# Performance work log

Measured on AMD Instinct MI355X. Metric: run time of the kernel, lower is better.

## Reference

```python
import jax, jax.numpy as jnp
import numpy as np

H = 32  # hidden size (hardcoded in source module)

def setup_inputs() -> dict:
    key = jax.random.key(0)
    ks = jax.random.split(key, 7)
    s = 1.0 / np.sqrt(H)  # PyTorch LSTM/Linear init scale
    return {
        "x":    jax.random.normal(ks[0], (8192, 512, 1), dtype=jnp.float32),
        "W_ih": jax.random.uniform(ks[1], (4 * H, 1), minval=-s, maxval=s, dtype=jnp.float32),
        "W_hh": jax.random.uniform(ks[2], (4 * H, H), minval=-s, maxval=s, dtype=jnp.float32),
        "b_ih": jax.random.uniform(ks[3], (4 * H,), minval=-s, maxval=s, dtype=jnp.float32),
        "b_hh": jax.random.uniform(ks[4], (4 * H,), minval=-s, maxval=s, dtype=jnp.float32),
        "W_fc": jax.random.uniform(ks[5], (1, H), minval=-s, maxval=s, dtype=jnp.float32),
        "b_fc": jax.random.uniform(ks[6], (1,), minval=-s, maxval=s, dtype=jnp.float32),
    }

def reference(x, W_ih, W_hh, b_ih, b_hh, W_fc, b_fc):
    B = x.shape[0]
    # Precompute input projections for all timesteps: [B, T, 4H]
    xg = jnp.einsum('bti,gi->btg', x, W_ih) + (b_ih + b_hh)
    xg_t = jnp.swapaxes(xg, 0, 1)  # [T, B, 4H] for scan over time

    def step(carry, xgt):
        h, c = carry
        gates = xgt + h @ W_hh.T           # [B, 4H]
        i, f, g, o = jnp.split(gates, 4, axis=-1)  # PyTorch gate order i,f,g,o
        i = jax.nn.sigmoid(i)
        f = jax.nn.sigmoid(f)
        g = jnp.tanh(g)
        o = jax.nn.sigmoid(o)
        c = f * c + i * g
        h = o * jnp.tanh(c)
        return (h, c), None

    h0 = jnp.zeros((B, H), dtype=x.dtype)
    c0 = jnp.zeros((B, H), dtype=x.dtype)
    (h_last, _), _ = jax.lax.scan(step, (h0, c0), xg_t)
    # Final linear head on last timestep hidden state: [B, output_size]
    return h_last @ W_fc.T + b_fc
```

## Files before the change

kernel.cpp:

```cpp
#include <hip/hip_runtime.h>
#include <hip/hip_bf16.h>


#define TT 512
#define HH 32
#define L2E 1.44269504088896340736f

typedef short bf16x8 __attribute__((ext_vector_type(8)));
typedef float f32x4 __attribute__((ext_vector_type(4)));

__device__ __forceinline__ short f2bf(float f) {
    unsigned u = __float_as_uint(f);
    u = (u + 0x7FFFu + ((u >> 16) & 1u)) >> 16;
    return (short)u;
}
__device__ __forceinline__ float bf2f(short s) {
    return __uint_as_float(((unsigned)(unsigned short)s) << 16);
}
__device__ __forceinline__ float fastrcp(float x) { return __builtin_amdgcn_rcpf(x); }
__device__ __forceinline__ float exp2f_(float x) { return __builtin_amdgcn_exp2f(x); }

#define XROW 132

__launch_bounds__(256, 2)
__global__ void lstm_kernel(const float* __restrict__ x,
                            const float* __restrict__ W_ih,
                            const float* __restrict__ W_hh,
                            const float* __restrict__ b_ih,
                            const float* __restrict__ b_hh,
                            const float* __restrict__ W_fc,
                            const float* __restrict__ b_fc,
                            float* __restrict__ out) {
    __shared__ short hhp[2][512];
    __shared__ short hlp[2][512];
    __shared__ float xbuf[16 * XROW];

    const int tid  = threadIdx.x;
    const int lane = tid & 63;
    const int w    = tid >> 6;
    const int c    = lane & 15;
    const int q    = lane >> 4;
    const int base = blockIdx.x * 16;

    const int gate = c & 3;
    const float asc = (gate == 2) ? (2.0f * L2E) : (-L2E);
    const int wrow0 = gate * 32 + 8 * (c >> 2);
    bf16x8 wah[2], wal[2];
    #pragma unroll
    for (int tt = 0; tt < 2; ++tt) {
        const int t8 = 2 * w + tt;
        #pragma unroll
        for (int j = 0; j < 8; ++j) {
            const float wf = W_hh[(wrow0 + t8) * HH + 8 * q + j] * asc;
            const short hi = f2bf(wf);
            wah[tt][j] = hi;
            wal[tt][j] = f2bf(wf - bf2f(hi));
        }
    }

    float wihs[2][4];
    f32x4 bcs[2];
    #pragma unroll
    for (int tt = 0; tt < 2; ++tt) {
        const int u = 8 * q + 2 * w + tt;
        #pragma unroll
        for (int r = 0; r < 4; ++r) {
            const float sc = (r == 2) ? (2.0f * L2E) : (-L2E);
            wihs[tt][r] = W_ih[32 * r + u] * sc;
            bcs[tt][r]  = (b_ih[32 * r + u] + b_hh[32 * r + u]) * sc;
        }
    }

    #pragma unroll
    for (int i = tid; i < 512; i += 256) { hhp[0][i] = 0; hlp[0][i] = 0; }

    float cs[2] = {0.f, 0.f};

    const int xrow = tid >> 4;
    const int xj4  = (tid & 15) * 4;

    const int rdo = q * 128 + c * 8;
    const int wro = q * 128 + c * 8 + 2 * w;

    #define STEP(t, RP, WP)                                                   \
    {                                                                         \
        const bf16x8 bh = *(const bf16x8*)&hhp[RP][rdo];                      \
        const bf16x8 bl = *(const bf16x8*)&hlp[RP][rdo];                      \
        const float xc = xbuf[c * XROW + ((t) & 127)];                        \
        f32x4 acc[2];                                                         \
        _Pragma("unroll")                                                     \
        for (int tt = 0; tt < 2; ++tt) {                                      \
            f32x4 a = bcs[tt];                                                \
            a = __builtin_amdgcn_mfma_f32_16x16x32_bf16(wah[tt], bh, a, 0,0,0);\
            a = __builtin_amdgcn_mfma_f32_16x16x32_bf16(wah[tt], bl, a, 0,0,0);\
            a = __builtin_amdgcn_mfma_f32_16x16x32_bf16(wal[tt], bh, a, 0,0,0);\
            acc[tt] = a;                                                      \
        }                                                                     \
        float hv[2];                                                          \
        _Pragma("unroll")                                                     \
        for (int tt = 0; tt < 2; ++tt) {                                      \
            const float Ei = exp2f_(acc[tt][0] + wihs[tt][0] * xc);           \
            const float Ef = exp2f_(acc[tt][1] + wihs[tt][1] * xc);           \
            const float G  = exp2f_(acc[tt][2] + wihs[tt][2] * xc);           \
            const float Eo = exp2f_(acc[tt][3] + wihs[tt][3] * xc);           \
            const float aig = (1.f + Ei) * (G + 1.f);                         \
            const float af  = 1.f + Ef;                                       \
            const float num = cs[tt] * aig + (G - 1.f) * af;                  \
            const float cn  = num * fastrcp(af * aig);                        \
            cs[tt] = cn;                                                      \
            float yc = cn * (2.0f * L2E);                                     \
            yc = fminf(60.f, fmaxf(-60.f, yc));                               \
            const float C = exp2f_(yc);                                       \
            hv[tt] = (C - 1.f) * fastrcp((C + 1.f) * (1.f + Eo));             \
        }                                                                     \
        union { __hip_bfloat162 b; int i; } ph, pl;                           \
        ph.b = __float22bfloat162_rn(make_float2(hv[0], hv[1]));              \
        const float h0h = bf2f((short)(ph.i & 0xFFFF));                       \
        const float h1h = bf2f((short)((unsigned)ph.i >> 16));                \
        pl.b = __float22bfloat162_rn(make_float2(hv[0] - h0h, hv[1] - h1h));  \
        *(int*)&hhp[WP][wro] = ph.i;                                          \
        *(int*)&hlp[WP][wro] = pl.i;                                          \
        __syncthreads();                                                      \
    }

    for (int t = 0; t < TT; t += 2) {
        if ((t & 127) == 0) {
            #pragma unroll
            for (int s = 0; s < 2; ++s) {
                const float4 v = *(const float4*)&x[(base + xrow) * TT + t + xj4 + 64 * s];
                *(float4*)&xbuf[xrow * XROW + xj4 + 64 * s] = v;
            }
            __syncthreads();
        }
        STEP(t,     0, 1);
        STEP(t + 1, 1, 0);
    }

    if (tid < 16) {
        float s = b_fc[0];
        #pragma unroll
        for (int u = 0; u < 32; ++u) {
            const int off = (u >> 3) * 128 + tid * 8 + (u & 7);
            s += (bf2f(hhp[0][off]) + bf2f(hlp[0][off])) * W_fc[u];
        }
        out[base + tid] = s;
    }
}

extern "C" void kernel_launch(void* const* d_in, const int* in_sizes, int n_in,
                              void* d_out, int out_size, void* d_ws, size_t ws_size,
                              hipStream_t stream) {
    const float* x    = (const float*)d_in[0];
    const float* W_ih = (const float*)d_in[1];
    const float* W_hh = (const float*)d_in[2];
    const float* b_ih = (const float*)d_in[3];
    const float* b_hh = (const float*)d_in[4];
    const float* W_fc = (const float*)d_in[5];
    const float* b_fc = (const float*)d_in[6];
    float* out = (float*)d_out;

    const int B = 8192;
    lstm_kernel<<<B / 16, 256, 0, stream>>>(x, W_ih, W_hh, b_ih, b_hh,
                                            W_fc, b_fc, out);
}
```

Measured before the change: 282.9 us.

## Process two 16-row batch groups per block to interleave independent recurrences

Each block now handles 32 batch rows as two independent 16-row groups, issuing the MFMAs for both groups before the gate math. The aim is to give each wave two independent dependency chains per timestep, hiding MFMA and transcendental latency, while halving the number of __syncthreads per sequence row. Launch bounds drop to one block per CU-slot and the grid halves to 256 blocks, which lowers occupancy and may leave many CUs on a 256-CU part idle or underused.

```diff
diff --git a/kernel.cpp b/kernel.cpp
--- a/kernel.cpp
+++ b/kernel.cpp
@@ -21,8 +21,9 @@
 __device__ __forceinline__ float exp2f_(float x) { return __builtin_amdgcn_exp2f(x); }
 
 #define XROW 132
+#define XSZ  (16 * XROW)
 
-__launch_bounds__(256, 2)
+__launch_bounds__(256, 1)
 __global__ void lstm_kernel(const float* __restrict__ x,
                             const float* __restrict__ W_ih,
                             const float* __restrict__ W_hh,
@@ -31,16 +32,16 @@
                             const float* __restrict__ W_fc,
                             const float* __restrict__ b_fc,
                             float* __restrict__ out) {
-    __shared__ short hhp[2][512];
-    __shared__ short hlp[2][512];
-    __shared__ float xbuf[16 * XROW];
+    __shared__ short hhp[2][2][512];
+    __shared__ short hlp[2][2][512];
+    __shared__ float xbuf[2][XSZ];
 
     const int tid  = threadIdx.x;
     const int lane = tid & 63;
     const int w    = tid >> 6;
     const int c    = lane & 15;
     const int q    = lane >> 4;
-    const int base = blockIdx.x * 16;
+    const int base = blockIdx.x * 32;
 
     const int gate = c & 3;
     const float asc = (gate == 2) ? (2.0f * L2E) : (-L2E);
@@ -72,63 +73,79 @@
     }
 
     #pragma unroll
-    for (int i = tid; i < 512; i += 256) { hhp[0][i] = 0; hlp[0][i] = 0; }
+    for (int i = tid; i < 512; i += 256) {
+        hhp[0][0][i] = 0; hlp[0][0][i] = 0;
+        hhp[1][0][i] = 0; hlp[1][0][i] = 0;
+    }
 
-    float cs[2] = {0.f, 0.f};
-
-    const int xrow = tid >> 4;
-    const int xj4  = (tid & 15) * 4;
+    float cs[2][2] = {{0.f, 0.f}, {0.f, 0.f}};
 
     const int rdo = q * 128 + c * 8;
-    const int wro = q * 128 + c * 8 + 2 * w;
+    const int wro = rdo + 2 * w;
 
     #define STEP(t, RP, WP)                                                   \
     {                                                                         \
-        const bf16x8 bh = *(const bf16x8*)&hhp[RP][rdo];                      \
-        const bf16x8 bl = *(const bf16x8*)&hlp[RP][rdo];                      \
-        const float xc = xbuf[c * XROW + ((t) & 127)];                        \
-        f32x4 acc[2];                                                         \
+        bf16x8 bhv[2], blv[2];                                                \
+        float xc[2];                                                          \
         _Pragma("unroll")                                                     \
-        for (int tt = 0; tt < 2; ++tt) {                                      \
-            f32x4 a = bcs[tt];                                                \
-            a = __builtin_amdgcn_mfma_f32_16x16x32_bf16(wah[tt], bh, a, 0,0,0);\
-            a = __builtin_amdgcn_mfma_f32_16x16x32_bf16(wah[tt], bl, a, 0,0,0);\
-            a = __builtin_amdgcn_mfma_f32_16x16x32_bf16(wal[tt], bh, a, 0,0,0);\
-            acc[tt] = a;                                                      \
+        for (int g = 0; g < 2; ++g) {                                         \
+            bhv[g] = *(const bf16x8*)&hhp[g][RP][rdo];                        \
+            blv[g] = *(const bf16x8*)&hlp[g][RP][rdo];                        \
+            xc[g]  = xbuf[g][c * XROW + ((t) & 127)];                         \
         }                                                                     \
-        float hv[2];                                                          \
+        f32x4 acc[2][2];                                                      \
         _Pragma("unroll")                                                     \
-        for (int tt = 0; tt < 2; ++tt) {                                      \
-            const float Ei = exp2f_(acc[tt][0] + wihs[tt][0] * xc);           \
-            const float Ef = exp2f_(acc[tt][1] + wihs[tt][1] * xc);           \
-            const float G  = exp2f_(acc[tt][2] + wihs[tt][2] * xc);           \
-            const float Eo = exp2f_(acc[tt][3] + wihs[tt][3] * xc);           \
-            const float aig = (1.f + Ei) * (G + 1.f);                         \
-            const float af  = 1.f + Ef;                                       \
-            const float num = cs[tt] * aig + (G - 1.f) * af;                  \
-            const float cn  = num * fastrcp(af * aig);                        \
-            cs[tt] = cn;                                                      \
-            float yc = cn * (2.0f * L2E);                                     \
-            yc = fminf(60.f, fmaxf(-60.f, yc));                               \
-            const float C = exp2f_(yc);                                       \
-            hv[tt] = (C - 1.f) * fastrcp((C + 1.f) * (1.f + Eo));             \
+        for (int g = 0; g < 2; ++g) {                                         \
+            _Pragma("unroll")                                                 \
+            for (int tt = 0; tt < 2; ++tt) {                                  \
+                f32x4 a = bcs[tt];                                            \
+                a = __builtin_amdgcn_mfma_f32_16x16x32_bf16(wah[tt], bhv[g], a, 0,0,0); \
+                a = __builtin_amdgcn_mfma_f32_16x16x32_bf16(wah[tt], blv[g], a, 0,0,0); \
+                a = __builtin_amdgcn_mfma_f32_16x16x32_bf16(wal[tt], bhv[g], a, 0,0,0); \
+                acc[g][tt] = a;                                               \
+            }                                                                 \
         }                                                                     \
-        union { __hip_bfloat162 b; int i; } ph, pl;                           \
-        ph.b = __float22bfloat162_rn(make_float2(hv[0], hv[1]));              \
-        const float h0h = bf2f((short)(ph.i & 0xFFFF));                       \
-        const float h1h = bf2f((short)((unsigned)ph.i >> 16));                \
-        pl.b = __float22bfloat162_rn(make_float2(hv[0] - h0h, hv[1] - h1h));  \
-        *(int*)&hhp[WP][wro] = ph.i;                                          \
-        *(int*)&hlp[WP][wro] = pl.i;                                          \
+        _Pragma("unroll")                                                     \
+        for (int g = 0; g < 2; ++g) {                                         \
+            float hv[2];                                                      \
+            _Pragma("unroll")                                                 \
+            for (int tt = 0; tt < 2; ++tt) {                                  \
+                const float Ei = exp2f_(acc[g][tt][0] + wihs[tt][0] * xc[g]); \
+                const float Ef = exp2f_(acc[g][tt][1] + wihs[tt][1] * xc[g]); \
+                const float G  = exp2f_(acc[g][tt][2] + wihs[tt][2] * xc[g]); \
+                const float Eo = exp2f_(acc[g][tt][3] + wihs[tt][3] * xc[g]); \
+                const float aig = (1.f + Ei) * (G + 1.f);                     \
+                const float af  = 1.f + Ef;                                   \
+                const float num = cs[g][tt] * aig + (G - 1.f) * af;           \
+                const float cn  = num * fastrcp(af * aig);                    \
+                cs[g][tt] = cn;                                               \
+                float yc = cn * (2.0f * L2E);                                 \
+                yc = fminf(60.f, fmaxf(-60.f, yc));                           \
+                const float C = exp2f_(yc);                                   \
+                hv[tt] = (C - 1.f) * fastrcp((C + 1.f) * (1.f + Eo));         \
+            }                                                                 \
+            union { __hip_bfloat162 b; int i; } ph, pl;                       \
+            ph.b = __float22bfloat162_rn(make_float2(hv[0], hv[1]));          \
+            const float h0h = bf2f((short)(ph.i & 0xFFFF));                   \
+            const float h1h = bf2f((short)((unsigned)ph.i >> 16));            \
+            pl.b = __float22bfloat162_rn(make_float2(hv[0] - h0h, hv[1] - h1h)); \
+            *(int*)&hhp[g][WP][wro] = ph.i;                                   \
+            *(int*)&hlp[g][WP][wro] = pl.i;                                   \
+        }                                                                     \
         __syncthreads();                                                      \
     }
 
     for (int t = 0; t < TT; t += 2) {
         if ((t & 127) == 0) {
             #pragma unroll
-            for (int s = 0; s < 2; ++s) {
-                const float4 v = *(const float4*)&x[(base + xrow) * TT + t + xj4 + 64 * s];
-                *(float4*)&xbuf[xrow * XROW + xj4 + 64 * s] = v;
+            for (int s = 0; s < 4; ++s) {
+                const int lin = tid + 256 * s;
+                const int g   = lin >> 9;
+                const int row = (lin >> 5) & 15;
+                const int j4  = (lin & 31) * 4;
+                const float4 v =
+                    *(const float4*)&x[(base + g * 16 + row) * TT + t + j4];
+                *(float4*)&xbuf[g][row * XROW + j4] = v;
             }
             __syncthreads();
         }
@@ -136,14 +153,16 @@
         STEP(t + 1, 1, 0);
     }
 
-    if (tid < 16) {
+    if (tid < 32) {
+        const int g  = tid >> 4;
+        const int bb = tid & 15;
         float s = b_fc[0];
         #pragma unroll
         for (int u = 0; u < 32; ++u) {
-            const int off = (u >> 3) * 128 + tid * 8 + (u & 7);
-            s += (bf2f(hhp[0][off]) + bf2f(hlp[0][off])) * W_fc[u];
+            const int off = (u >> 3) * 128 + bb * 8 + (u & 7);
+            s += (bf2f(hhp[g][0][off]) + bf2f(hlp[g][0][off])) * W_fc[u];
         }
-        out[base + tid] = s;
+        out[base + g * 16 + bb] = s;
     }
 }
 
@@ -160,6 +179,6 @@
     float* out = (float*)d_out;
 
     const int B = 8192;
-    lstm_kernel<<<B / 16, 256, 0, stream>>>(x, W_ih, W_hh, b_ih, b_hh,
+    lstm_kernel<<<B / 32, 256, 0, stream>>>(x, W_ih, W_hh, b_ih, b_hh,
                                             W_fc, b_fc, out);
 }
```

Measured after the change: 322.8 us. +14.1%, slower.

## Split MFMA dependency chain and swizzle h write slots to avoid LDS bank conflicts

Applied to the files above, without the earlier changes.

The three chained MFMAs per gate tile become two independent chains: hi*hi from zero, and a second chain seeded with the input projection plus bias that adds the lo corrections. The two partial results are summed afterwards, which shortens the serial MFMA latency on the recurrent critical path and moves the x-projection FMA off the post-MFMA path. The hidden-state write offsets and the W_hh column order are XOR-swizzled by quad so the per-step 32-bit LDS writes spread across banks, and the final FC read uses the same permutation. The cost is extra vector adds and a slightly different floating-point summation order.

```diff
diff --git a/kernel.cpp b/kernel.cpp
--- a/kernel.cpp
+++ b/kernel.cpp
@@ -51,7 +51,8 @@
         const int t8 = 2 * w + tt;
         #pragma unroll
         for (int j = 0; j < 8; ++j) {
-            const float wf = W_hh[(wrow0 + t8) * HH + 8 * q + j] * asc;
+            const int u = 8 * q + (j ^ (2 * q));
+            const float wf = W_hh[(wrow0 + t8) * HH + u] * asc;
             const short hi = f2bf(wf);
             wah[tt][j] = hi;
             wal[tt][j] = f2bf(wf - bf2f(hi));
@@ -80,7 +81,7 @@
     const int xj4  = (tid & 15) * 4;
 
     const int rdo = q * 128 + c * 8;
-    const int wro = q * 128 + c * 8 + 2 * w;
+    const int wro = rdo + ((2 * w) ^ (2 * q));
 
     #define STEP(t, RP, WP)                                                   \
     {                                                                         \
@@ -90,19 +91,23 @@
         f32x4 acc[2];                                                         \
         _Pragma("unroll")                                                     \
         for (int tt = 0; tt < 2; ++tt) {                                      \
-            f32x4 a = bcs[tt];                                                \
-            a = __builtin_amdgcn_mfma_f32_16x16x32_bf16(wah[tt], bh, a, 0,0,0);\
-            a = __builtin_amdgcn_mfma_f32_16x16x32_bf16(wah[tt], bl, a, 0,0,0);\
-            a = __builtin_amdgcn_mfma_f32_16x16x32_bf16(wal[tt], bh, a, 0,0,0);\
-            acc[tt] = a;                                                      \
+            f32x4 ci;                                                         \
+            _Pragma("unroll")                                                 \
+            for (int r = 0; r < 4; ++r) ci[r] = wihs[tt][r] * xc + bcs[tt][r];\
+            f32x4 a1 = {0.f, 0.f, 0.f, 0.f};                                  \
+            a1 = __builtin_amdgcn_mfma_f32_16x16x32_bf16(wah[tt], bh, a1, 0,0,0);\
+            f32x4 a2 = __builtin_amdgcn_mfma_f32_16x16x32_bf16(wal[tt], bh, ci, 0,0,0);\
+            a2 = __builtin_amdgcn_mfma_f32_16x16x32_bf16(wah[tt], bl, a2, 0,0,0);\
+            _Pragma("unroll")                                                 \
+            for (int r = 0; r < 4; ++r) acc[tt][r] = a1[r] + a2[r];           \
         }                                                                     \
         float hv[2];                                                          \
         _Pragma("unroll")                                                     \
         for (int tt = 0; tt < 2; ++tt) {                                      \
-            const float Ei = exp2f_(acc[tt][0] + wihs[tt][0] * xc);           \
-            const float Ef = exp2f_(acc[tt][1] + wihs[tt][1] * xc);           \
-            const float G  = exp2f_(acc[tt][2] + wihs[tt][2] * xc);           \
-            const float Eo = exp2f_(acc[tt][3] + wihs[tt][3] * xc);           \
+            const float Ei = exp2f_(acc[tt][0]);                              \
+            const float Ef = exp2f_(acc[tt][1]);                              \
+            const float G  = exp2f_(acc[tt][2]);                              \
+            const float Eo = exp2f_(acc[tt][3]);                              \
             const float aig = (1.f + Ei) * (G + 1.f);                         \
             const float af  = 1.f + Ef;                                       \
             const float num = cs[tt] * aig + (G - 1.f) * af;                  \
@@ -140,7 +145,8 @@
         float s = b_fc[0];
         #pragma unroll
         for (int u = 0; u < 32; ++u) {
-            const int off = (u >> 3) * 128 + tid * 8 + (u & 7);
+            const int qb = u >> 3;
+            const int off = qb * 128 + tid * 8 + ((u & 7) ^ (2 * qb));
             s += (bf2f(hhp[0][off]) + bf2f(hlp[0][off])) * W_fc[u];
         }
         out[base + tid] = s;
```

Measured after the change: 290.4 us. 2.6% more time.

## Interleave two batch groups per block and use split fp16 MFMA recurrence

Applied to the files above, without the earlier changes.

Each block now handles 32 sequences as two 16-row groups whose time steps are staggered, so one group's gate nonlinearities overlap the other group's MFMA work. The recurrence switches from bf16 hi/lo with three MFMAs per tile to fp16 weights with a hi/lo split of h only, two MFMAs per tile. Each of 8 waves owns one tile instead of two. The x input is double-buffered across 128-step chunks, and an XOR swizzle is applied to the h writes to reduce LDS bank conflicts. The trade-off is lower weight precision (fp16 instead of bf16 hi+lo) and fewer, larger blocks.

```diff
diff --git a/kernel.cpp b/kernel.cpp
--- a/kernel.cpp
+++ b/kernel.cpp
@@ -1,28 +1,19 @@
 #include <hip/hip_runtime.h>
-#include <hip/hip_bf16.h>
 
 
 #define TT 512
 #define HH 32
 #define L2E 1.44269504088896340736f
 
-typedef short bf16x8 __attribute__((ext_vector_type(8)));
+typedef _Float16 f16x8 __attribute__((ext_vector_type(8)));
 typedef float f32x4 __attribute__((ext_vector_type(4)));
 
-__device__ __forceinline__ short f2bf(float f) {
-    unsigned u = __float_as_uint(f);
-    u = (u + 0x7FFFu + ((u >> 16) & 1u)) >> 16;
-    return (short)u;
-}
-__device__ __forceinline__ float bf2f(short s) {
-    return __uint_as_float(((unsigned)(unsigned short)s) << 16);
-}
 __device__ __forceinline__ float fastrcp(float x) { return __builtin_amdgcn_rcpf(x); }
 __device__ __forceinline__ float exp2f_(float x) { return __builtin_amdgcn_exp2f(x); }
 
 #define XROW 132
 
-__launch_bounds__(256, 2)
+__launch_bounds__(512)
 __global__ void lstm_kernel(const float* __restrict__ x,
                             const float* __restrict__ W_ih,
                             const float* __restrict__ W_hh,
@@ -31,119 +22,137 @@
                             const float* __restrict__ W_fc,
                             const float* __restrict__ b_fc,
                             float* __restrict__ out) {
-    __shared__ short hhp[2][512];
-    __shared__ short hlp[2][512];
-    __shared__ float xbuf[16 * XROW];
+    __shared__ _Float16 hh[2][512];
+    __shared__ _Float16 hl[2][512];
+    __shared__ float xbuf[2][2][16 * XROW];
 
     const int tid  = threadIdx.x;
     const int lane = tid & 63;
     const int w    = tid >> 6;
     const int c    = lane & 15;
     const int q    = lane >> 4;
-    const int base = blockIdx.x * 16;
+    const int base = blockIdx.x * 32;
 
     const int gate = c & 3;
     const float asc = (gate == 2) ? (2.0f * L2E) : (-L2E);
-    const int wrow0 = gate * 32 + 8 * (c >> 2);
-    bf16x8 wah[2], wal[2];
+    const int arow = gate * 32 + 8 * (c >> 2) + w;
+    f16x8 wah;
     #pragma unroll
-    for (int tt = 0; tt < 2; ++tt) {
-        const int t8 = 2 * w + tt;
-        #pragma unroll
-        for (int j = 0; j < 8; ++j) {
-            const float wf = W_hh[(wrow0 + t8) * HH + 8 * q + j] * asc;
-            const short hi = f2bf(wf);
-            wah[tt][j] = hi;
-            wal[tt][j] = f2bf(wf - bf2f(hi));
-        }
+    for (int j = 0; j < 8; ++j) {
+        const int u = 8 * q + (j ^ (2 * q));
+        wah[j] = (_Float16)(W_hh[arow * HH + u] * asc);
     }
 
-    float wihs[2][4];
-    f32x4 bcs[2];
+    const int uu = 8 * q + w;
+    f32x4 wihs, bcs;
     #pragma unroll
-    for (int tt = 0; tt < 2; ++tt) {
-        const int u = 8 * q + 2 * w + tt;
-        #pragma unroll
-        for (int r = 0; r < 4; ++r) {
-            const float sc = (r == 2) ? (2.0f * L2E) : (-L2E);
-            wihs[tt][r] = W_ih[32 * r + u] * sc;
-            bcs[tt][r]  = (b_ih[32 * r + u] + b_hh[32 * r + u]) * sc;
-        }
+    for (int r = 0; r < 4; ++r) {
+        const float sc = (r == 2) ? (2.0f * L2E) : (-L2E);
+        wihs[r] = W_ih[32 * r + uu] * sc;
+        bcs[r]  = (b_ih[32 * r + uu] + b_hh[32 * r + uu]) * sc;
     }
 
-    #pragma unroll
-    for (int i = tid; i < 512; i += 256) { hhp[0][i] = 0; hlp[0][i] = 0; }
+    hh[0][tid] = (_Float16)0.f; hl[0][tid] = (_Float16)0.f;
+    hh[1][tid] = (_Float16)0.f; hl[1][tid] = (_Float16)0.f;
 
-    float cs[2] = {0.f, 0.f};
+    float csA = 0.f, csB = 0.f;
 
-    const int xrow = tid >> 4;
-    const int xj4  = (tid & 15) * 4;
+    const float xB0 = x[(base + 16 + c) * TT + 0];
+    f32x4 accB = wihs * xB0 + bcs;
+    f32x4 accA;
 
     const int rdo = q * 128 + c * 8;
-    const int wro = q * 128 + c * 8 + 2 * w;
+    const int wro = rdo + (w ^ (2 * q));
 
-    #define STEP(t, RP, WP)                                                   \
-    {                                                                         \
-        const bf16x8 bh = *(const bf16x8*)&hhp[RP][rdo];                      \
-        const bf16x8 bl = *(const bf16x8*)&hlp[RP][rdo];                      \
-        const float xc = xbuf[c * XROW + ((t) & 127)];                        \
-        f32x4 acc[2];                                                         \
-        _Pragma("unroll")                                                     \
-        for (int tt = 0; tt < 2; ++tt) {                                      \
-            f32x4 a = bcs[tt];                                                \
-            a = __builtin_amdgcn_mfma_f32_16x16x32_bf16(wah[tt], bh, a, 0,0,0);\
-            a = __builtin_amdgcn_mfma_f32_16x16x32_bf16(wah[tt], bl, a, 0,0,0);\
-            a = __builtin_amdgcn_mfma_f32_16x16x32_bf16(wal[tt], bh, a, 0,0,0);\
-            acc[tt] = a;                                                      \
-        }                                                                     \
-        float hv[2];                                                          \
-        _Pragma("unroll")                                                     \
-        for (int tt = 0; tt < 2; ++tt) {                                      \
-            const float Ei = exp2f_(acc[tt][0] + wihs[tt][0] * xc);           \
-            const float Ef = exp2f_(acc[tt][1] + wihs[tt][1] * xc);           \
-            const float G  = exp2f_(acc[tt][2] + wihs[tt][2] * xc);           \
-            const float Eo = exp2f_(acc[tt][3] + wihs[tt][3] * xc);           \
+    const int xrow = tid >> 5;
+    const int xj4  = (tid & 31) * 4;
+
+    #define CELL(ACC, CS, H)                                                  \
+        {                                                                     \
+            const float Ei = exp2f_(ACC[0]);                                  \
+            const float Ef = exp2f_(ACC[1]);                                  \
+            const float G  = exp2f_(ACC[2]);                                  \
+            const float Eo = exp2f_(ACC[3]);                                  \
             const float aig = (1.f + Ei) * (G + 1.f);                         \
             const float af  = 1.f + Ef;                                       \
-            const float num = cs[tt] * aig + (G - 1.f) * af;                  \
-            const float cn  = num * fastrcp(af * aig);                        \
-            cs[tt] = cn;                                                      \
+            const float cn  = (CS * aig + (G - 1.f) * af) * fastrcp(af * aig);\
+            CS = cn;                                                          \
             float yc = cn * (2.0f * L2E);                                     \
             yc = fminf(60.f, fmaxf(-60.f, yc));                               \
             const float C = exp2f_(yc);                                       \
-            hv[tt] = (C - 1.f) * fastrcp((C + 1.f) * (1.f + Eo));             \
-        }                                                                     \
-        union { __hip_bfloat162 b; int i; } ph, pl;                           \
-        ph.b = __float22bfloat162_rn(make_float2(hv[0], hv[1]));              \
-        const float h0h = bf2f((short)(ph.i & 0xFFFF));                       \
-        const float h1h = bf2f((short)((unsigned)ph.i >> 16));                \
-        pl.b = __float22bfloat162_rn(make_float2(hv[0] - h0h, hv[1] - h1h));  \
-        *(int*)&hhp[WP][wro] = ph.i;                                          \
-        *(int*)&hlp[WP][wro] = pl.i;                                          \
-        __syncthreads();                                                      \
-    }
+            H = (C - 1.f) * fastrcp((C + 1.f) * (1.f + Eo));                  \
+        }
 
-    for (int t = 0; t < TT; t += 2) {
-        if ((t & 127) == 0) {
-            #pragma unroll
-            for (int s = 0; s < 2; ++s) {
-                const float4 v = *(const float4*)&x[(base + xrow) * TT + t + xj4 + 64 * s];
-                *(float4*)&xbuf[xrow * XROW + xj4 + 64 * s] = v;
+    for (int m = 0; m < TT; ++m) {
+        if ((m & 127) == 0) {
+            const int kt = m >> 7;
+            if (kt == 0) {
+                #pragma unroll
+                for (int k = 0; k < 2; ++k) {
+                    #pragma unroll
+                    for (int g = 0; g < 2; ++g) {
+                        const float4 v = *(const float4*)
+                            &x[(base + g * 16 + xrow) * TT + 128 * k + xj4];
+                        *(float4*)&xbuf[k][g][xrow * XROW + xj4] = v;
+                    }
+                }
+            } else if (kt < 3) {
+                #pragma unroll
+                for (int g = 0; g < 2; ++g) {
+                    const float4 v = *(const float4*)
+                        &x[(base + g * 16 + xrow) * TT + 128 * (kt + 1) + xj4];
+                    *(float4*)&xbuf[(kt + 1) & 1][g][xrow * XROW + xj4] = v;
+                }
             }
             __syncthreads();
         }
-        STEP(t,     0, 1);
-        STEP(t + 1, 1, 0);
+
+        {
+            const f16x8 bhA = *(const f16x8*)&hh[0][rdo];
+            const f16x8 blA = *(const f16x8*)&hl[0][rdo];
+            const float xA  = xbuf[(m >> 7) & 1][0][c * XROW + (m & 127)];
+
+            float hB;
+            CELL(accB, csB, hB);
+            const _Float16 hB16 = (_Float16)hB;
+            hh[1][wro] = hB16;
+            hl[1][wro] = (_Float16)(hB - (float)hB16);
+
+            f32x4 ci = wihs * xA + bcs;
+            ci = __builtin_amdgcn_mfma_f32_16x16x32_f16(wah, blA, ci, 0, 0, 0);
+            accA = __builtin_amdgcn_mfma_f32_16x16x32_f16(wah, bhA, ci, 0, 0, 0);
+        }
+        __syncthreads();
+
+        {
+            const f16x8 bhB = *(const f16x8*)&hh[1][rdo];
+            const f16x8 blB = *(const f16x8*)&hl[1][rdo];
+            const int tn = (m + 1 < TT) ? (m + 1) : (TT - 1);
+            const float xB = xbuf[(tn >> 7) & 1][1][c * XROW + (tn & 127)];
+
+            float hA;
+            CELL(accA, csA, hA);
+            const _Float16 hA16 = (_Float16)hA;
+            hh[0][wro] = hA16;
+            hl[0][wro] = (_Float16)(hA - (float)hA16);
+
+            f32x4 ci = wihs * xB + bcs;
+            ci = __builtin_amdgcn_mfma_f32_16x16x32_f16(wah, blB, ci, 0, 0, 0);
+            accB = __builtin_amdgcn_mfma_f32_16x16x32_f16(wah, bhB, ci, 0, 0, 0);
+        }
+        __syncthreads();
     }
 
-    if (tid < 16) {
+    if (tid < 32) {
+        const int g  = tid >> 4;
+        const int bb = tid & 15;
         float s = b_fc[0];
         #pragma unroll
         for (int u = 0; u < 32; ++u) {
-            const int off = (u >> 3) * 128 + tid * 8 + (u & 7);
-            s += (bf2f(hhp[0][off]) + bf2f(hlp[0][off])) * W_fc[u];
+            const int off = (u >> 3) * 128 + bb * 8 + ((u & 7) ^ (2 * (u >> 3)));
+            s += ((float)hh[g][off] + (float)hl[g][off]) * W_fc[u];
         }
-        out[base + tid] = s;
+        out[base + g * 16 + bb] = s;
     }
 }
 
@@ -160,6 +169,6 @@
     float* out = (float*)d_out;
 
     const int B = 8192;
-    lstm_kernel<<<B / 16, 256, 0, stream>>>(x, W_ih, W_hh, b_ih, b_hh,
+    lstm_kernel<<<B / 32, 512, 0, stream>>>(x, W_ih, W_hh, b_ih, b_hh,
                                             W_fc, b_fc, out);
 }
```

New measurement: 322.5 us. 1.14x slower.
